# Performance work log

Measured on AMD Instinct MI355X. Metric: run time of the kernel, lower is better.

## Reference

```python
import jax, jax.numpy as jnp
import numpy as np

K = 7          # kernel_size
PAD = K // 2
NAZ, NEL = 12, 5
HID = 64
IC = 2         # input_channels == num_instruments
OC = 2         # output_channels (stereo)
EPS = 1e-5


def conv1d_same(x, w, b):
    # x: (N, Cin, T), w: (Cout, Cin, K) -> (N, Cout, T); cross-correlation like torch
    y = jax.lax.conv_general_dilated(x, w, (1,), 'SAME',
                                     dimension_numbers=('NCH', 'OIH', 'NCH'))
    return y + b[None, :, None]


def batchnorm(x, g, bt):
    # training-mode BatchNorm1d: biased batch stats over (N, T)
    mean = x.mean(axis=(0, 2), keepdims=True)
    var = x.var(axis=(0, 2), keepdims=True)
    return (x - mean) * jax.lax.rsqrt(var + EPS) * g[None, :, None] + bt[None, :, None]


def lrelu(x):
    return jnp.where(x >= 0, x, 0.2 * x)


def setup_inputs() -> dict:
    key = jax.random.key(0)
    ks = jax.random.split(key, 16)
    d = {}
    d['x'] = jax.random.normal(ks[0], (8, IC, 131072), dtype=jnp.float32)
    # spatial_param_net
    d['W1'] = jax.random.normal(ks[1], (HID, IC, K), dtype=jnp.float32) * 0.1
    d['b1'] = jnp.zeros((HID,), jnp.float32)
    d['g1'] = jnp.ones((HID,), jnp.float32)
    d['be1'] = jnp.zeros((HID,), jnp.float32)
    d['W2'] = jax.random.normal(ks[2], (2 * HID, HID, K), dtype=jnp.float32) * 0.05
    d['b2'] = jnp.zeros((2 * HID,), jnp.float32)
    d['g2'] = jnp.ones((2 * HID,), jnp.float32)
    d['be2'] = jnp.zeros((2 * HID,), jnp.float32)
    d['W3'] = jax.random.normal(ks[3], (IC * 3, 2 * HID, K), dtype=jnp.float32) * 0.05
    d['b3'] = jnp.zeros((IC * 3,), jnp.float32)
    # HRTF table: (num_azimuth*num_elevation, output_channels, K)
    d['hrtf'] = jax.random.normal(ks[4], (NAZ * NEL, OC, K), dtype=jnp.float32)
    # binaural_renderer (first conv in-channels = input_channels = 2)
    d['RW1'] = jax.random.normal(ks[5], (HID, IC, K), dtype=jnp.float32) * 0.1
    d['rb1'] = jnp.zeros((HID,), jnp.float32)
    d['rg1'] = jnp.ones((HID,), jnp.float32)
    d['rbe1'] = jnp.zeros((HID,), jnp.float32)
    d['RW2'] = jax.random.normal(ks[6], (2 * HID, HID, K), dtype=jnp.float32) * 0.05
    d['rb2'] = jnp.zeros((2 * HID,), jnp.float32)
    d['rg2'] = jnp.ones((2 * HID,), jnp.float32)
    d['rbe2'] = jnp.zeros((2 * HID,), jnp.float32)
    d['RW3'] = jax.random.normal(ks[7], (OC, 2 * HID, K), dtype=jnp.float32) * 0.05
    d['rb3'] = jnp.zeros((OC,), jnp.float32)
    return d


def reference(x, W1, b1, g1, be1, W2, b2, g2, be2, W3, b3, hrtf,
              RW1, rb1, rg1, rbe1, RW2, rb2, rg2, rbe2, RW3, rb3):
    B, I, T = x.shape
    # spatial parameter network
    h = lrelu(batchnorm(conv1d_same(x, W1, b1), g1, be1))
    h = lrelu(batchnorm(conv1d_same(h, W2, b2), g2, be2))
    sp = jnp.tanh(conv1d_same(h, W3, b3)).reshape(B, I, 3, T)
    # only t=0 of azimuth/elevation/distance is used (matches torch loop)
    az = (sp[:, :, 0, 0] + 1.0) * 0.5 * (NAZ - 1)
    el = (sp[:, :, 1, 0] + 1.0) * 0.5 * (NEL - 1)
    dist = (sp[:, :, 2, 0] + 1.0) * 0.5 * 0.9 + 0.1      # (B, I)
    az_i = jnp.clip(az.astype(jnp.int32), 0, NAZ - 1)
    el_i = jnp.clip(el.astype(jnp.int32), 0, NEL - 1)
    idx = el_i * NAZ + az_i                               # (B, I)
    wg = hrtf[idx]                                        # (B, I, OC, K) gathered filters
    # per-(b,i) conv1d with its gathered HRTF filter, scale by distance, sum over instruments
    xp = jnp.pad(x, ((0, 0), (0, 0), (PAD, PAD)))
    windows = jnp.stack([xp[:, :, k:k + T] for k in range(K)], axis=2)  # (B, I, K, T)
    summed = jnp.einsum('bikt,bick,bi->bct', windows, wg, dist)          # (B, OC, T)
    # binaural renderer
    h = lrelu(batchnorm(conv1d_same(summed, RW1, rb1), rg1, rbe1))
    h = lrelu(batchnorm(conv1d_same(h, RW2, rb2), rg2, rbe2))
    return jnp.tanh(conv1d_same(h, RW3, rb3))
```

## Files before the change

kernel.cpp:

```cpp
#include <hip/hip_runtime.h>
#include <hip/hip_fp16.h>
#include <cstddef>


#define TLEN 131072
#define NB 8
#define NICH 2
#define NHID 64
#define NH2 128
#define EPSV 1e-5f
#define CNTF 1048576.0f
#define FT 120
#define FGRID 1093
#define XCH 2048

typedef _Float16 f16x8 __attribute__((ext_vector_type(8)));
typedef float f32x4 __attribute__((ext_vector_type(4)));

__device__ __forceinline__ float lrelu(float v) { return fmaxf(v, 0.2f * v); }
__device__ __forceinline__ unsigned short h16(float v) {
  return __half_as_ushort(__float2half(v));
}
__device__ __forceinline__ float fh16(unsigned short u) {
  return __half2float(__ushort_as_half(u));
}
__device__ __forceinline__ float ftanh(float x) {
  float e = __expf(2.f * x);
  return 1.f - 2.f / (e + 1.f);
}

__global__ __launch_bounds__(256) void prep_weights(
    const float* __restrict__ W2c, const float* __restrict__ RW2c,
    const float* __restrict__ RW3c,
    const float* __restrict__ W1c, const float* __restrict__ RW1c,
    unsigned short* __restrict__ w2sp, unsigned short* __restrict__ w2re,
    unsigned short* __restrict__ w3g,
    unsigned short* __restrict__ w1sp, unsigned short* __restrict__ w1re)
{
  int e = blockIdx.x * 256 + threadIdx.x;
  if (e < 114688) {
    int e2 = (e >= 57344) ? e - 57344 : e;
    int frag = e2 >> 9, within = e2 & 511;
    int c = frag >> 3, mt = frag & 7;
    int mn = within >> 5, kk = within & 31;
    int o = mt * 16 + mn;
    int tap = c >> 1, ch = (c & 1) * 32 + kk;
    const float* src = (e >= 57344) ? RW2c : W2c;
    unsigned short* dst = (e >= 57344) ? w2re : w2sp;
    dst[e2] = h16(src[(o * 64 + ch) * 7 + tap]);
  } else if (e < 116736) {
    int e2 = e - 114688;
    int c = e2 >> 9, within = e2 & 511;
    int m = within >> 5, kk = within & 31;
    int ch = c * 32 + kk;
    w3g[e2] = (m < 14) ? h16(RW3c[((m / 7) * 128 + ch) * 7 + (m % 7)])
                       : (unsigned short)0;
  } else if (e < 120832) {
    int e2 = e - 116736;
    int which = (e2 >= 2048);
    int e3 = e2 & 2047;
    int m = e3 >> 9, w = e3 & 511;
    int mn = w >> 5, K = w & 31;
    int i = K >> 4, kk = K & 15;
    const float* src = which ? RW1c : W1c;
    unsigned short* dst = which ? w1re : w1sp;
    dst[e3] = (kk < 7) ? h16(src[(m * 16 + mn) * 14 + i * 7 + kk])
                       : (unsigned short)0;
  }
}

__global__ __launch_bounds__(256) void xcorr_stats(
    const float* __restrict__ z, float* __restrict__ partials)
{
  const int b = blockIdx.x >> 6;
  const int t0 = (blockIdx.x & 63) * XCH;
  __shared__ float zs[2][XCH + 8];
  __shared__ float redx[4][30];
  for (int i = 0; i < 2; ++i)
    for (int j = threadIdx.x; j < XCH + 7; j += 256) {
      int tg = t0 + j;
      zs[i][j] = (tg < TLEN) ? z[(b * 2 + i) * TLEN + tg] : 0.f;
    }
  __syncthreads();

  float acc[30];
  #pragma unroll
  for (int q = 0; q < 30; ++q) acc[q] = 0.f;
  const int tb = threadIdx.x * 8;
  #pragma unroll
  for (int tt = 0; tt < 8; ++tt) {
    int j = tb + tt;
    float z0 = zs[0][j], z1 = zs[1][j];
    acc[28] += z0; acc[29] += z1;
    #pragma unroll
    for (int d = 0; d < 7; ++d) {
      float a0 = zs[0][j + d], a1 = zs[1][j + d];
      acc[d]      += z0 * a0;
      acc[7 + d]  += z0 * a1;
      acc[14 + d] += z1 * a0;
      acc[21 + d] += z1 * a1;
    }
  }
  #pragma unroll
  for (int q = 0; q < 30; ++q)
    #pragma unroll
    for (int m = 1; m <= 32; m <<= 1)
      acc[q] += __shfl_xor(acc[q], m, 64);
  const int lane = threadIdx.x & 63, wv = threadIdx.x >> 6;
  if (lane == 0)
    #pragma unroll
    for (int q = 0; q < 30; ++q) redx[wv][q] = acc[q];
  __syncthreads();
  if (threadIdx.x < 30)
    partials[blockIdx.x * 30 + threadIdx.x] =
        redx[0][threadIdx.x] + redx[1][threadIdx.x] +
        redx[2][threadIdx.x] + redx[3][threadIdx.x];
}

__global__ __launch_bounds__(256) void assemble_coef1(
    const float* __restrict__ partials, int nblocks,
    const float* __restrict__ W1c, const float* __restrict__ b1c,
    const float* __restrict__ g, const float* __restrict__ be,
    float* __restrict__ coef)
{
  __shared__ float R[30];
  __shared__ float pr[8][30];
  __shared__ float w1s[64 * 14];
  for (int e = threadIdx.x; e < 64 * 14; e += 256) w1s[e] = W1c[e];
  if (threadIdx.x < 240) {
    int q = threadIdx.x % 30, chunk = threadIdx.x / 30;
    float s = 0.f;
    for (int j = chunk; j < nblocks; j += 8) s += partials[j * 30 + q];
    pr[chunk][q] = s;
  }
  __syncthreads();
  if (threadIdx.x < 30) {
    float s = 0.f;
    #pragma unroll
    for (int c = 0; c < 8; ++c) s += pr[c][threadIdx.x];
    R[threadIdx.x] = s;
  }
  __syncthreads();
  if (threadIdx.x < 64) {
    int o = threadIdx.x;
    const float* w = &w1s[o * 14];
    float b1v = b1c[o];
    float sy = 0.f;
    #pragma unroll
    for (int i = 0; i < 2; ++i)
      #pragma unroll
      for (int k = 0; k < 7; ++k) sy += w[i * 7 + k] * R[28 + i];
    float syy = 0.f;
    #pragma unroll
    for (int i = 0; i < 2; ++i)
      #pragma unroll
      for (int k = 0; k < 7; ++k) {
        float wv = w[i * 7 + k];
        #pragma unroll
        for (int i2 = 0; i2 < 2; ++i2)
          #pragma unroll
          for (int k2 = 0; k2 < 7; ++k2) {
            int d = k2 - k;
            float r = (d >= 0) ? R[i * 14 + i2 * 7 + d]
                               : R[i2 * 14 + i * 7 - d];
            syy += wv * w[i2 * 7 + k2] * r;
          }
      }
    float S1 = CNTF * b1v + sy;
    float S2 = 2.f * b1v * S1 - CNTF * b1v * b1v + syy;
    float mean = S1 / CNTF;
    float var = S2 / CNTF - mean * mean;
    float a = g[o] * rsqrtf(var + EPSV);
    coef[o] = a;
    coef[64 + o] = be[o] - mean * a;
  }
}

__global__ __launch_bounds__(256) void reduce_coef(
    const float* __restrict__ partials, int nblocks, int C,
    const float* __restrict__ bso,
    const float* __restrict__ g, const float* __restrict__ be,
    float* __restrict__ coef)
{
  const int c = blockIdx.x;
  float s = 0.f, ss = 0.f;
  for (int j = threadIdx.x; j < nblocks; j += 256) {
    s  += partials[j * 2 * C + c];
    ss += partials[j * 2 * C + C + c];
  }
  #pragma unroll
  for (int off = 32; off >= 1; off >>= 1) {
    s  += __shfl_down(s, off, 64);
    ss += __shfl_down(ss, off, 64);
  }
  __shared__ float rs[4], rss[4];
  const int lane = threadIdx.x & 63, wv = threadIdx.x >> 6;
  if (lane == 0) { rs[wv] = s; rss[wv] = ss; }
  __syncthreads();
  if (threadIdx.x == 0) {
    float st  = rs[0] + rs[1] + rs[2] + rs[3];
    float sst = rss[0] + rss[1] + rss[2] + rss[3];
    float mean = st / CNTF;
    float var  = sst / CNTF - mean * mean;
    float a = g[c] * rsqrtf(var + EPSV);
    float d = be[c] - mean * a;
    coef[c] = a;
    coef[C + c] = d;
    coef[2 * C + c] = d + a * bso[c];
  }
}

__device__ __forceinline__ void stage_x(
    int t0, int xoff, const float* __restrict__ xin, int b, float* xs)
{
  for (int e = threadIdx.x; e < 2 * 168; e += 256) {
    int i = e / 168, j = e % 168;
    int tg = t0 - xoff + j;
    xs[e] = (tg >= 0 && tg < TLEN) ? xin[(b * NICH + i) * TLEN + tg] : 0.f;
  }
}

template<int HOF>
__device__ __forceinline__ void h1_mfma(
    int t0, const float* xs, unsigned short* xw,
    const unsigned short* __restrict__ w1f,
    const float* __restrict__ coef1, const float* __restrict__ b1c,
    unsigned short* h1f)
{
  for (int e = threadIdx.x; e < 144 * 2; e += 256) {
    int n = e >> 1, i = e & 1;
    const float* xp = &xs[i * 168 + n];
    unsigned short hv[7];
    #pragma unroll
    for (int kk = 0; kk < 7; ++kk) hv[kk] = h16(xp[kk]);
    *(uint4*)(xw + n * 32 + i * 16) = make_uint4(
        hv[0] | ((unsigned)hv[1] << 16), hv[2] | ((unsigned)hv[3] << 16),
        hv[4] | ((unsigned)hv[5] << 16), (unsigned)hv[6]);
    *(uint4*)(xw + n * 32 + i * 16 + 8) = make_uint4(0, 0, 0, 0);
  }
  __syncthreads();

  const int lane = threadIdx.x & 63;
  const int wv = threadIdx.x >> 6;
  const int mn = lane & 15, quad = lane >> 4;
  f16x8 A1 = *(const f16x8*)(w1f + wv * 512 + mn * 32 + quad * 8);
  f32x4 acc1[9];
  #pragma unroll
  for (int nt = 0; nt < 9; ++nt) {
    f32x4 z = {0.f, 0.f, 0.f, 0.f};
    acc1[nt] = z;
  }
  #pragma unroll
  for (int nt = 0; nt < 9; ++nt) {
    f16x8 bb = *(const f16x8*)(xw + (nt * 16 + mn) * 32 + quad * 8);
    acc1[nt] = __builtin_amdgcn_mfma_f32_16x16x32_f16(A1, bb, acc1[nt], 0, 0, 0);
  }
  const int ch0 = wv * 16 + quad * 4;
  float a1v[4], dd[4];
  #pragma unroll
  for (int r = 0; r < 4; ++r) {
    a1v[r] = coef1[ch0 + r];
    dd[r]  = coef1[64 + ch0 + r] + a1v[r] * b1c[ch0 + r];
  }
  #pragma unroll
  for (int nt = 0; nt < 9; ++nt) {
    int n = nt * 16 + mn;
    int t = t0 - HOF + n;
    bool ok = (t >= 0) && (t < TLEN);
    unsigned us[4];
    #pragma unroll
    for (int r = 0; r < 4; ++r) {
      float v = lrelu(a1v[r] * acc1[nt][r] + dd[r]);
      us[r] = h16(ok ? v : 0.f);
    }
    *(uint2*)(h1f + n * 72 + ch0) =
        make_uint2(us[0] | (us[1] << 16), us[2] | (us[3] << 16));
  }
}

template<int SAVE>
__global__ __launch_bounds__(256, 4) void conv2_stats_mfma(
    const float* __restrict__ xin,
    const unsigned short* __restrict__ w1f, const float* __restrict__ b1c,
    const float* __restrict__ coef1,
    const unsigned short* __restrict__ w2f,
    const float* __restrict__ b2c,
    float* __restrict__ partials,
    unsigned short* __restrict__ h1out)
{
  const int b  = blockIdx.x >> 10;
  const int t0 = (blockIdx.x & 1023) * 128;

  __shared__ __align__(16) char smem[31296];
  unsigned short* h1f = (unsigned short*)smem;
  float* xs = (float*)(smem + 20736);
  unsigned short* xw = (unsigned short*)(smem + 22080);
  float* redS = (float*)smem;
  float* redSS= (float*)(smem + 8704);

  stage_x(t0, 6, xin, b, xs);
  __syncthreads();
  h1_mfma<3>(t0, xs, xw, w1f, coef1, b1c, h1f);
  __syncthreads();

  const int lane = threadIdx.x & 63;
  const int wv = threadIdx.x >> 6;
  const int mn = lane & 15, quad = lane >> 4;

  f32x4 acc[2][8];
  #pragma unroll
  for (int mt = 0; mt < 2; ++mt)
    #pragma unroll
    for (int nt = 0; nt < 8; ++nt) {
      f32x4 z = {0.f, 0.f, 0.f, 0.f};
      acc[mt][nt] = z;
    }

  f16x8 ca[2], na[2];
  auto loadA = [&](int c, f16x8 (&A)[2]) {
    #pragma unroll
    for (int mt = 0; mt < 2; ++mt)
      A[mt] = *(const f16x8*)(w2f + (c * 8 + wv * 2 + mt) * 512 + mn * 32 + quad * 8);
  };
  loadA(0, ca);
  #pragma unroll
  for (int c = 0; c < 14; ++c) {
    if (c < 13) loadA(c + 1, na);
    const int tap = c >> 1;
    const int ch0 = (c & 1) * 32 + quad * 8;
    #pragma unroll
    for (int nt = 0; nt < 8; ++nt) {
      f16x8 bb = *(const f16x8*)(h1f + (nt * 16 + mn + tap) * 72 + ch0);
      acc[0][nt] = __builtin_amdgcn_mfma_f32_16x16x32_f16(ca[0], bb, acc[0][nt], 0, 0, 0);
      acc[1][nt] = __builtin_amdgcn_mfma_f32_16x16x32_f16(ca[1], bb, acc[1][nt], 0, 0, 0);
    }
    ca[0] = na[0]; ca[1] = na[1];
  }

  if (SAVE == 1) {
    for (int e = threadIdx.x; e < 1024; e += 256) {
      int row = e >> 3, c8 = (e & 7) * 8;
      *(uint4*)(h1out + ((size_t)(b * TLEN + t0 + row) * 64 + c8)) =
          *(const uint4*)(h1f + (row + 3) * 72 + c8);
    }
  }
  __syncthreads();

  #pragma unroll
  for (int mt = 0; mt < 2; ++mt)
    #pragma unroll
    for (int r = 0; r < 4; ++r) {
      int o = (wv * 2 + mt) * 16 + quad * 4 + r;
      float bo = b2c[o];
      float s = 0.f, ss = 0.f;
      #pragma unroll
      for (int nt = 0; nt < 8; ++nt) {
        float v = acc[mt][nt][r] + bo;
        s += v; ss += v * v;
      }
      redS[o * 17 + mn] = s;
      redSS[o * 17 + mn] = ss;
    }
  __syncthreads();
  {
    int o = threadIdx.x & 127;
    const float* src = (threadIdx.x < 128) ? redS : redSS;
    float s = 0.f;
    #pragma unroll
    for (int j = 0; j < 16; ++j) s += src[o * 17 + j];
    partials[blockIdx.x * 256 + threadIdx.x] = s;
  }
}

__global__ __launch_bounds__(256) void finalize_spatial(
    const float* __restrict__ x,
    const float* __restrict__ W1c, const float* __restrict__ b1c,
    const float* __restrict__ coef1,
    const float* __restrict__ W2c, const float* __restrict__ b2c,
    const float* __restrict__ coef2,
    const float* __restrict__ W3c, const float* __restrict__ b3c,
    const float* __restrict__ hrtf, float* __restrict__ wgbuf)
{
  __shared__ float xl[NB * 2 * 16];
  __shared__ float h1l[NB * 64 * 10];
  __shared__ float h2l[NB * NH2 * 4];
  __shared__ float sp[48];
  const int tid = threadIdx.x;
  {
    int bb = tid >> 5, i = (tid >> 4) & 1, j = tid & 15;
    int t = j - 6;
    xl[tid] = (t >= 0) ? x[(bb * 2 + i) * TLEN + t] : 0.f;
  }
  __syncthreads();
  for (int e = tid; e < NB * 64; e += 256) {
    int bb = e >> 6, ch = e & 63;
    float a1 = coef1[ch], d1 = coef1[64 + ch], bo = b1c[ch];
    for (int tt = 0; tt < 10; ++tt) {
      float acc = bo;
      #pragma unroll
      for (int i2 = 0; i2 < 2; ++i2)
        #pragma unroll
        for (int k = 0; k < 7; ++k)
          acc += xl[(bb * 2 + i2) * 16 + tt + k] * W1c[ch * 14 + i2 * 7 + k];
      float v = lrelu(a1 * acc + d1);
      h1l[(bb * 64 + ch) * 10 + tt] = (tt >= 3) ? v : 0.f;
    }
  }
  __syncthreads();
  for (int e = tid; e < NB * NH2; e += 256) {
    int bb = e >> 7, o = e & 127;
    float a2 = coef2[o], d2 = coef2[NH2 + o], bo = b2c[o];
    float acc[4] = {bo, bo, bo, bo};
    for (int i = 0; i < 64; ++i)
      #pragma unroll
      for (int k = 0; k < 7; ++k) {
        float w = W2c[(o * 64 + i) * 7 + k];
        #pragma unroll
        for (int t = 0; t < 4; ++t)
          acc[t] += h1l[(bb * 64 + i) * 10 + t + k] * w;
      }
    #pragma unroll
    for (int t = 0; t < 4; ++t)
      h2l[(bb * NH2 + o) * 4 + t] = lrelu(a2 * acc[t] + d2);
  }
  __syncthreads();
  if (tid < 48) {
    int bb = tid / 6, c3 = tid % 6;
    float acc = b3c[c3];
    for (int c = 0; c < NH2; ++c)
      #pragma unroll
      for (int k = 3; k < 7; ++k)
        acc += h2l[(bb * NH2 + c) * 4 + (k - 3)] * W3c[(c3 * NH2 + c) * 7 + k];
    sp[tid] = tanhf(acc);
  }
  __syncthreads();
  if (tid < 16) {
    int bb = tid >> 1, i = tid & 1;
    float az = (sp[bb * 6 + i * 3 + 0] + 1.f) * 0.5f * 11.f;
    float el = (sp[bb * 6 + i * 3 + 1] + 1.f) * 0.5f * 4.f;
    float dist = (sp[bb * 6 + i * 3 + 2] + 1.f) * 0.5f * 0.9f + 0.1f;
    int azi = min(max((int)az, 0), 11);
    int eli = min(max((int)el, 0), 4);
    int idx = eli * 12 + azi;
    for (int e = 0; e < 14; ++e)
      wgbuf[(bb * 2 + i) * 14 + e] = hrtf[idx * 14 + e] * dist;
  }
}

__global__ __launch_bounds__(256) void mix_kernel(
    const float* __restrict__ x, const float* __restrict__ wgbuf,
    float* __restrict__ summed)
{
  const int b = blockIdx.x >> 7;
  const int t0 = (blockIdx.x & 127) * 1024 + threadIdx.x * 4;
  float wv[2][2][7];
  #pragma unroll
  for (int i = 0; i < 2; ++i)
    #pragma unroll
    for (int c = 0; c < 2; ++c)
      #pragma unroll
      for (int k = 0; k < 7; ++k)
        wv[i][c][k] = wgbuf[(b * 2 + i) * 14 + c * 7 + k];
  float acc[2][4] = {{0.f, 0.f, 0.f, 0.f}, {0.f, 0.f, 0.f, 0.f}};
  #pragma unroll
  for (int i = 0; i < 2; ++i) {
    float xl[12];
    #pragma unroll
    for (int j = 0; j < 12; ++j) {
      int tg = t0 - 4 + j;
      xl[j] = (tg >= 0 && tg < TLEN) ? x[(b * 2 + i) * TLEN + tg] : 0.f;
    }
    #pragma unroll
    for (int c = 0; c < 2; ++c)
      #pragma unroll
      for (int k = 0; k < 7; ++k)
        #pragma unroll
        for (int tt = 0; tt < 4; ++tt)
          acc[c][tt] += xl[tt + k + 1] * wv[i][c][k];
  }
  #pragma unroll
  for (int c = 0; c < 2; ++c)
    *reinterpret_cast<float4*>(&summed[(b * 2 + c) * TLEN + t0]) =
        make_float4(acc[c][0], acc[c][1], acc[c][2], acc[c][3]);
}

__device__ __forceinline__ void final_tail(
    int b, int t0, f32x4 (&acc)[2][8],
    const float* __restrict__ coef2,
    const unsigned short* __restrict__ w3g, const float* __restrict__ rb3c,
    unsigned short* h2t, unsigned short* dq, float* __restrict__ out)
{
  const int lane = threadIdx.x & 63;
  const int wv = threadIdx.x >> 6;
  const int mn = lane & 15, quad = lane >> 4;

  float a2v[2][4], dd2[2][4];
  #pragma unroll
  for (int mt = 0; mt < 2; ++mt)
    #pragma unroll
    for (int r = 0; r < 4; ++r) {
      int o = (wv * 2 + mt) * 16 + quad * 4 + r;
      a2v[mt][r] = coef2[o];
      dd2[mt][r] = coef2[2 * NH2 + o];
    }
  __syncthreads();

  #pragma unroll
  for (int nt = 0; nt < 8; ++nt) {
    int jp = nt * 16 + mn;
    int t = t0 - 3 + jp;
    bool ok = (t >= 0) && (t < TLEN);
    #pragma unroll
    for (int mt = 0; mt < 2; ++mt) {
      int obase = (wv * 2 + mt) * 16 + quad * 4;
      unsigned us[4];
      #pragma unroll
      for (int r = 0; r < 4; ++r) {
        float v = lrelu(a2v[mt][r] * acc[mt][nt][r] + dd2[mt][r]);
        us[r] = h16(ok ? v : 0.f);
      }
      *(uint2*)(h2t + jp * 136 + obase) =
          make_uint2(us[0] | (us[1] << 16), us[2] | (us[3] << 16));
    }
  }
  __syncthreads();

  const int nt0 = wv * 2;
  f32x4 acc3[2];
  #pragma unroll
  for (int i = 0; i < 2; ++i) {
    f32x4 z = {0.f, 0.f, 0.f, 0.f};
    acc3[i] = z;
  }
  #pragma unroll
  for (int c = 0; c < 4; ++c) {
    f16x8 A3 = *(const f16x8*)(w3g + c * 512 + mn * 32 + quad * 8);
    #pragma unroll
    for (int i = 0; i < 2; ++i) {
      f16x8 bb = *(const f16x8*)(h2t + ((nt0 + i) * 16 + mn) * 136 + c * 32 + quad * 8);
      acc3[i] = __builtin_amdgcn_mfma_f32_16x16x32_f16(A3, bb, acc3[i], 0, 0, 0);
    }
  }
  #pragma unroll
  for (int i = 0; i < 2; ++i) {
    int n = (nt0 + i) * 16 + mn;
    unsigned us[4];
    #pragma unroll
    for (int r = 0; r < 4; ++r) us[r] = h16(acc3[i][r]);
    *(uint2*)(dq + n * 20 + quad * 4) =
        make_uint2(us[0] | (us[1] << 16), us[2] | (us[3] << 16));
  }
  __syncthreads();

  {
    int tid = threadIdx.x;
    if (tid < 240) {
      int oc = (tid >= FT) ? 1 : 0;
      int u = tid - oc * FT;
      float s = rb3c[oc];
      #pragma unroll
      for (int tap = 0; tap < 7; ++tap)
        s += fh16(dq[(u + tap) * 20 + oc * 7 + tap]);
      int t = t0 + u;
      if (t < TLEN) out[(b * 2 + oc) * TLEN + t] = ftanh(s);
    }
  }
}

__device__ __forceinline__ void conv2_loop(
    const unsigned short* h1f, const unsigned short* __restrict__ w2f,
    f32x4 (&acc)[2][8])
{
  const int lane = threadIdx.x & 63;
  const int wv = threadIdx.x >> 6;
  const int mn = lane & 15, quad = lane >> 4;
  #pragma unroll
  for (int mt = 0; mt < 2; ++mt)
    #pragma unroll
    for (int nt = 0; nt < 8; ++nt) {
      f32x4 z = {0.f, 0.f, 0.f, 0.f};
      acc[mt][nt] = z;
    }
  f16x8 ca[2], na[2];
  auto loadA = [&](int c, f16x8 (&A)[2]) {
    #pragma unroll
    for (int mt = 0; mt < 2; ++mt)
      A[mt] = *(const f16x8*)(w2f + (c * 8 + wv * 2 + mt) * 512 + mn * 32 + quad * 8);
  };
  loadA(0, ca);
  #pragma unroll
  for (int c = 0; c < 14; ++c) {
    if (c < 13) loadA(c + 1, na);
    const int tap = c >> 1;
    const int ch0 = (c & 1) * 32 + quad * 8;
    #pragma unroll
    for (int nt = 0; nt < 8; ++nt) {
      f16x8 bb = *(const f16x8*)(h1f + (nt * 16 + mn + tap) * 72 + ch0);
      acc[0][nt] = __builtin_amdgcn_mfma_f32_16x16x32_f16(ca[0], bb, acc[0][nt], 0, 0, 0);
      acc[1][nt] = __builtin_amdgcn_mfma_f32_16x16x32_f16(ca[1], bb, acc[1][nt], 0, 0, 0);
    }
    ca[0] = na[0]; ca[1] = na[1];
  }
}

__global__ __launch_bounds__(256, 4) void conv2_final_mfma(
    const float* __restrict__ xin,
    const unsigned short* __restrict__ w1f, const float* __restrict__ b1c,
    const float* __restrict__ coef1,
    const unsigned short* __restrict__ w2f,
    const float* __restrict__ coef2,
    const unsigned short* __restrict__ w3g, const float* __restrict__ rb3c,
    float* __restrict__ out)
{
  const int b  = blockIdx.y;
  const int t0 = blockIdx.x * FT;

  __shared__ __align__(16) char smem[39936];
  unsigned short* h1f = (unsigned short*)smem;
  float* xs = (float*)(smem + 20736);
  unsigned short* xw = (unsigned short*)(smem + 22080);
  unsigned short* h2t = (unsigned short*)smem;
  unsigned short* dq  = (unsigned short*)(smem + 34816);

  stage_x(t0, 9, xin, b, xs);
  __syncthreads();
  h1_mfma<6>(t0, xs, xw, w1f, coef1, b1c, h1f);
  __syncthreads();

  f32x4 acc[2][8];
  conv2_loop(h1f, w2f, acc);
  final_tail(b, t0, acc, coef2, w3g, rb3c, h2t, dq, out);
}

__global__ __launch_bounds__(256, 4) void conv2_final_h1(
    const unsigned short* __restrict__ h1g,
    const unsigned short* __restrict__ w2f,
    const float* __restrict__ coef2,
    const unsigned short* __restrict__ w3g, const float* __restrict__ rb3c,
    float* __restrict__ out)
{
  const int b  = blockIdx.y;
  const int t0 = blockIdx.x * FT;

  __shared__ __align__(16) char smem[39936];
  unsigned short* h1f = (unsigned short*)smem;
  unsigned short* h2t = (unsigned short*)smem;
  unsigned short* dq  = (unsigned short*)(smem + 34816);

  for (int e = threadIdx.x; e < 144 * 8; e += 256) {
    int r = e >> 3, c8 = (e & 7) * 8;
    int t = t0 - 6 + r;
    uint4 v = make_uint4(0, 0, 0, 0);
    if (t >= 0 && t < TLEN)
      v = *(const uint4*)(h1g + ((size_t)(b * TLEN + t) * 64 + c8));
    *(uint4*)(h1f + r * 72 + c8) = v;
  }
  __syncthreads();

  f32x4 acc[2][8];
  conv2_loop(h1f, w2f, acc);
  final_tail(b, t0, acc, coef2, w3g, rb3c, h2t, dq, out);
}

extern "C" void kernel_launch(void* const* d_in, const int* in_sizes, int n_in,
                              void* d_out, int out_size, void* d_ws, size_t ws_size,
                              hipStream_t stream)
{
  (void)in_sizes; (void)n_in; (void)out_size;
  const float* x    = (const float*)d_in[0];
  const float* W1   = (const float*)d_in[1];
  const float* b1   = (const float*)d_in[2];
  const float* g1   = (const float*)d_in[3];
  const float* be1  = (const float*)d_in[4];
  const float* W2   = (const float*)d_in[5];
  const float* b2   = (const float*)d_in[6];
  const float* g2   = (const float*)d_in[7];
  const float* be2  = (const float*)d_in[8];
  const float* W3   = (const float*)d_in[9];
  const float* b3   = (const float*)d_in[10];
  const float* hrtf = (const float*)d_in[11];
  const float* RW1  = (const float*)d_in[12];
  const float* rb1  = (const float*)d_in[13];
  const float* rg1  = (const float*)d_in[14];
  const float* rbe1 = (const float*)d_in[15];
  const float* RW2  = (const float*)d_in[16];
  const float* rb2  = (const float*)d_in[17];
  const float* rg2  = (const float*)d_in[18];
  const float* rbe2 = (const float*)d_in[19];
  const float* RW3  = (const float*)d_in[20];
  const float* rb3  = (const float*)d_in[21];
  float* out = (float*)d_out;

  float* partialsB = (float*)d_out;

  char* ws = (char*)d_ws;
  float* partialsA      = (float*)(ws + 0);
  float* summed         = (float*)(ws + 524288);
  float* coef1          = (float*)(ws + 8912896);
  float* coef2          = (float*)(ws + 8913408);
  float* coefR1         = (float*)(ws + 8914944);
  float* coefR2         = (float*)(ws + 8915456);
  float* wgbuf          = (float*)(ws + 8916992);
  unsigned short* w2sp  = (unsigned short*)(ws + 8918016);
  unsigned short* w2re  = (unsigned short*)(ws + 9032704);
  unsigned short* w3g   = (unsigned short*)(ws + 9147392);
  unsigned short* w1sp  = (unsigned short*)(ws + 9151488);
  unsigned short* w1re  = (unsigned short*)(ws + 9155584);
  unsigned short* h1g   = (unsigned short*)(ws + 16777216);
  const size_t WS_NEEDED_MID = 16777216ull + 134217728ull;
  const bool mid = ws_size >= WS_NEEDED_MID;

  prep_weights<<<472, 256, 0, stream>>>(W2, RW2, RW3, W1, RW1,
                                        w2sp, w2re, w3g, w1sp, w1re);
  xcorr_stats<<<512, 256, 0, stream>>>(x, partialsA);
  assemble_coef1<<<1, 256, 0, stream>>>(partialsA, 512, W1, b1, g1, be1, coef1);
  conv2_stats_mfma<0><<<8192, 256, 0, stream>>>(x, w1sp, b1, coef1, w2sp,
                                                b2, partialsB, nullptr);
  reduce_coef<<<128, 256, 0, stream>>>(partialsB, 8192, 128, b2, g2, be2, coef2);
  finalize_spatial<<<1, 256, 0, stream>>>(x, W1, b1, coef1, W2, b2, coef2,
                                          W3, b3, hrtf, wgbuf);
  mix_kernel<<<1024, 256, 0, stream>>>(x, wgbuf, summed);
  xcorr_stats<<<512, 256, 0, stream>>>(summed, partialsA);
  assemble_coef1<<<1, 256, 0, stream>>>(partialsA, 512, RW1, rb1, rg1, rbe1, coefR1);
  if (mid) {
    conv2_stats_mfma<1><<<8192, 256, 0, stream>>>(summed, w1re, rb1, coefR1,
                                                  w2re, rb2, partialsB, h1g);
  } else {
    conv2_stats_mfma<0><<<8192, 256, 0, stream>>>(summed, w1re, rb1, coefR1,
                                                  w2re, rb2, partialsB, nullptr);
  }
  reduce_coef<<<128, 256, 0, stream>>>(partialsB, 8192, 128, rb2, rg2, rbe2, coefR2);
  if (mid) {
    conv2_final_h1<<<dim3(FGRID, NB), 256, 0, stream>>>(
        h1g, w2re, coefR2, w3g, rb3, out);
  } else {
    conv2_final_mfma<<<dim3(FGRID, NB), 256, 0, stream>>>(
        summed, w1re, rb1, coefR1, w2re, coefR2, w3g, rb3, out);
  }
}
```

Baseline: 655.4 us.

## Fuse HRTF mix with renderer input cross-correlation stats; parallelize spatial finalize

```diff
diff --git a/kernel.cpp b/kernel.cpp
--- a/kernel.cpp
+++ b/kernel.cpp
@@ -303,46 +303,46 @@
   h1_mfma<3>(t0, xs, xw, w1f, coef1, b1c, h1f);
   __syncthreads();
 
-  const int lane = threadIdx.x & 63;
-  const int wv = threadIdx.x >> 6;
-  const int mn = lane & 15, quad = lane >> 4;
-
-  f32x4 acc[2][8];
-  #pragma unroll
-  for (int mt = 0; mt < 2; ++mt)
-    #pragma unroll
-    for (int nt = 0; nt < 8; ++nt) {
-      f32x4 z = {0.f, 0.f, 0.f, 0.f};
-      acc[mt][nt] = z;
-    }
-
-  f16x8 ca[2], na[2];
-  auto loadA = [&](int c, f16x8 (&A)[2]) {
-    #pragma unroll
-    for (int mt = 0; mt < 2; ++mt)
-      A[mt] = *(const f16x8*)(w2f + (c * 8 + wv * 2 + mt) * 512 + mn * 32 + quad * 8);
-  };
-  loadA(0, ca);
-  #pragma unroll
-  for (int c = 0; c < 14; ++c) {
-    if (c < 13) loadA(c + 1, na);
-    const int tap = c >> 1;
-    const int ch0 = (c & 1) * 32 + quad * 8;
-    #pragma unroll
-    for (int nt = 0; nt < 8; ++nt) {
-      f16x8 bb = *(const f16x8*)(h1f + (nt * 16 + mn + tap) * 72 + ch0);
-      acc[0][nt] = __builtin_amdgcn_mfma_f32_16x16x32_f16(ca[0], bb, acc[0][nt], 0, 0, 0);
-      acc[1][nt] = __builtin_amdgcn_mfma_f32_16x16x32_f16(ca[1], bb, acc[1][nt], 0, 0, 0);
-    }
-    ca[0] = na[0]; ca[1] = na[1];
-  }
-
   if (SAVE == 1) {
     for (int e = threadIdx.x; e < 1024; e += 256) {
       int row = e >> 3, c8 = (e & 7) * 8;
       *(uint4*)(h1out + ((size_t)(b * TLEN + t0 + row) * 64 + c8)) =
           *(const uint4*)(h1f + (row + 3) * 72 + c8);
     }
+  }
+
+  const int lane = threadIdx.x & 63;
+  const int wv = threadIdx.x >> 6;
+  const int mn = lane & 15, quad = lane >> 4;
+
+  f32x4 acc[2][8];
+  #pragma unroll
+  for (int mt = 0; mt < 2; ++mt)
+    #pragma unroll
+    for (int nt = 0; nt < 8; ++nt) {
+      f32x4 z = {0.f, 0.f, 0.f, 0.f};
+      acc[mt][nt] = z;
+    }
+
+  f16x8 ca[2], na[2];
+  auto loadA = [&](int c, f16x8 (&A)[2]) {
+    #pragma unroll
+    for (int mt = 0; mt < 2; ++mt)
+      A[mt] = *(const f16x8*)(w2f + (c * 8 + wv * 2 + mt) * 512 + mn * 32 + quad * 8);
+  };
+  loadA(0, ca);
+  #pragma unroll
+  for (int c = 0; c < 14; ++c) {
+    if (c < 13) loadA(c + 1, na);
+    const int tap = c >> 1;
+    const int ch0 = (c & 1) * 32 + quad * 8;
+    #pragma unroll
+    for (int nt = 0; nt < 8; ++nt) {
+      f16x8 bb = *(const f16x8*)(h1f + (nt * 16 + mn + tap) * 72 + ch0);
+      acc[0][nt] = __builtin_amdgcn_mfma_f32_16x16x32_f16(ca[0], bb, acc[0][nt], 0, 0, 0);
+      acc[1][nt] = __builtin_amdgcn_mfma_f32_16x16x32_f16(ca[1], bb, acc[1][nt], 0, 0, 0);
+    }
+    ca[0] = na[0]; ca[1] = na[1];
   }
   __syncthreads();
 
@@ -381,19 +381,20 @@
     const float* __restrict__ W3c, const float* __restrict__ b3c,
     const float* __restrict__ hrtf, float* __restrict__ wgbuf)
 {
-  __shared__ float xl[NB * 2 * 16];
-  __shared__ float h1l[NB * 64 * 10];
-  __shared__ float h2l[NB * NH2 * 4];
-  __shared__ float sp[48];
+  const int bb = blockIdx.x;
+  __shared__ float xl[2 * 16];
+  __shared__ float h1l[64 * 10];
+  __shared__ float h2l[NH2 * 4];
+  __shared__ float sp[6];
   const int tid = threadIdx.x;
-  {
-    int bb = tid >> 5, i = (tid >> 4) & 1, j = tid & 15;
+  if (tid < 32) {
+    int i = tid >> 4, j = tid & 15;
     int t = j - 6;
     xl[tid] = (t >= 0) ? x[(bb * 2 + i) * TLEN + t] : 0.f;
   }
   __syncthreads();
-  for (int e = tid; e < NB * 64; e += 256) {
-    int bb = e >> 6, ch = e & 63;
+  if (tid < 64) {
+    int ch = tid;
     float a1 = coef1[ch], d1 = coef1[64 + ch], bo = b1c[ch];
     for (int tt = 0; tt < 10; ++tt) {
       float acc = bo;
@@ -401,14 +402,14 @@
       for (int i2 = 0; i2 < 2; ++i2)
         #pragma unroll
         for (int k = 0; k < 7; ++k)
-          acc += xl[(bb * 2 + i2) * 16 + tt + k] * W1c[ch * 14 + i2 * 7 + k];
+          acc += xl[i2 * 16 + tt + k] * W1c[ch * 14 + i2 * 7 + k];
       float v = lrelu(a1 * acc + d1);
-      h1l[(bb * 64 + ch) * 10 + tt] = (tt >= 3) ? v : 0.f;
-    }
-  }
-  __syncthreads();
-  for (int e = tid; e < NB * NH2; e += 256) {
-    int bb = e >> 7, o = e & 127;
+      h1l[ch * 10 + tt] = (tt >= 3) ? v : 0.f;
+    }
+  }
+  __syncthreads();
+  if (tid < NH2) {
+    int o = tid;
     float a2 = coef2[o], d2 = coef2[NH2 + o], bo = b2c[o];
     float acc[4] = {bo, bo, bo, bo};
     for (int i = 0; i < 64; ++i)
@@ -417,28 +418,28 @@
         float w = W2c[(o * 64 + i) * 7 + k];
         #pragma unroll
         for (int t = 0; t < 4; ++t)
-          acc[t] += h1l[(bb * 64 + i) * 10 + t + k] * w;
+          acc[t] += h1l[i * 10 + t + k] * w;
       }
     #pragma unroll
     for (int t = 0; t < 4; ++t)
-      h2l[(bb * NH2 + o) * 4 + t] = lrelu(a2 * acc[t] + d2);
-  }
-  __syncthreads();
-  if (tid < 48) {
-    int bb = tid / 6, c3 = tid % 6;
+      h2l[o * 4 + t] = lrelu(a2 * acc[t] + d2);
+  }
+  __syncthreads();
+  if (tid < 6) {
+    int c3 = tid;
     float acc = b3c[c3];
     for (int c = 0; c < NH2; ++c)
       #pragma unroll
       for (int k = 3; k < 7; ++k)
-        acc += h2l[(bb * NH2 + c) * 4 + (k - 3)] * W3c[(c3 * NH2 + c) * 7 + k];
-    sp[tid] = tanhf(acc);
-  }
-  __syncthreads();
-  if (tid < 16) {
-    int bb = tid >> 1, i = tid & 1;
-    float az = (sp[bb * 6 + i * 3 + 0] + 1.f) * 0.5f * 11.f;
-    float el = (sp[bb * 6 + i * 3 + 1] + 1.f) * 0.5f * 4.f;
-    float dist = (sp[bb * 6 + i * 3 + 2] + 1.f) * 0.5f * 0.9f + 0.1f;
+        acc += h2l[c * 4 + (k - 3)] * W3c[(c3 * NH2 + c) * 7 + k];
+    sp[c3] = tanhf(acc);
+  }
+  __syncthreads();
+  if (tid < 2) {
+    int i = tid;
+    float az = (sp[i * 3 + 0] + 1.f) * 0.5f * 11.f;
+    float el = (sp[i * 3 + 1] + 1.f) * 0.5f * 4.f;
+    float dist = (sp[i * 3 + 2] + 1.f) * 0.5f * 0.9f + 0.1f;
     int azi = min(max((int)az, 0), 11);
     int eli = min(max((int)el, 0), 4);
     int idx = eli * 12 + azi;
@@ -447,12 +448,15 @@
   }
 }
 
-__global__ __launch_bounds__(256) void mix_kernel(
+__global__ __launch_bounds__(256) void mix_xcorr(
     const float* __restrict__ x, const float* __restrict__ wgbuf,
-    float* __restrict__ summed)
-{
-  const int b = blockIdx.x >> 7;
-  const int t0 = (blockIdx.x & 127) * 1024 + threadIdx.x * 4;
+    float* __restrict__ summed, float* __restrict__ partials)
+{
+  const int b = blockIdx.x >> 6;
+  const int t0 = (blockIdx.x & 63) * XCH;
+  __shared__ float zs[2][XCH + 8];
+  __shared__ float redx[4][30];
+
   float wv[2][2][7];
   #pragma unroll
   for (int i = 0; i < 2; ++i)
@@ -461,27 +465,90 @@
       #pragma unroll
       for (int k = 0; k < 7; ++k)
         wv[i][c][k] = wgbuf[(b * 2 + i) * 14 + c * 7 + k];
-  float acc[2][4] = {{0.f, 0.f, 0.f, 0.f}, {0.f, 0.f, 0.f, 0.f}};
-  #pragma unroll
-  for (int i = 0; i < 2; ++i) {
-    float xl[12];
-    #pragma unroll
-    for (int j = 0; j < 12; ++j) {
-      int tg = t0 - 4 + j;
-      xl[j] = (tg >= 0 && tg < TLEN) ? x[(b * 2 + i) * TLEN + tg] : 0.f;
-    }
+
+  const int tb = threadIdx.x * 8;
+  {
+    float acc[2][8];
     #pragma unroll
     for (int c = 0; c < 2; ++c)
       #pragma unroll
-      for (int k = 0; k < 7; ++k)
+      for (int tt = 0; tt < 8; ++tt) acc[c][tt] = 0.f;
+    #pragma unroll
+    for (int i = 0; i < 2; ++i) {
+      float xl[14];
+      #pragma unroll
+      for (int j = 0; j < 14; ++j) {
+        int tg = t0 + tb - 3 + j;
+        xl[j] = (tg >= 0 && tg < TLEN) ? x[(b * 2 + i) * TLEN + tg] : 0.f;
+      }
+      #pragma unroll
+      for (int c = 0; c < 2; ++c)
         #pragma unroll
-        for (int tt = 0; tt < 4; ++tt)
-          acc[c][tt] += xl[tt + k + 1] * wv[i][c][k];
-  }
-  #pragma unroll
-  for (int c = 0; c < 2; ++c)
-    *reinterpret_cast<float4*>(&summed[(b * 2 + c) * TLEN + t0]) =
-        make_float4(acc[c][0], acc[c][1], acc[c][2], acc[c][3]);
+        for (int k = 0; k < 7; ++k)
+          #pragma unroll
+          for (int tt = 0; tt < 8; ++tt)
+            acc[c][tt] += xl[tt + k] * wv[i][c][k];
+    }
+    #pragma unroll
+    for (int c = 0; c < 2; ++c) {
+      #pragma unroll
+      for (int tt = 0; tt < 8; ++tt) zs[c][tb + tt] = acc[c][tt];
+      *reinterpret_cast<float4*>(&summed[(b * 2 + c) * TLEN + t0 + tb]) =
+          make_float4(acc[c][0], acc[c][1], acc[c][2], acc[c][3]);
+      *reinterpret_cast<float4*>(&summed[(b * 2 + c) * TLEN + t0 + tb + 4]) =
+          make_float4(acc[c][4], acc[c][5], acc[c][6], acc[c][7]);
+    }
+  }
+  if (threadIdx.x < 7) {
+    int t = t0 + XCH + threadIdx.x;
+    float s0 = 0.f, s1 = 0.f;
+    if (t < TLEN) {
+      #pragma unroll
+      for (int i = 0; i < 2; ++i)
+        #pragma unroll
+        for (int k = 0; k < 7; ++k) {
+          int tg = t + k - 3;
+          float xv = (tg >= 0 && tg < TLEN) ? x[(b * 2 + i) * TLEN + tg] : 0.f;
+          s0 += xv * wv[i][0][k];
+          s1 += xv * wv[i][1][k];
+        }
+    }
+    zs[0][XCH + threadIdx.x] = s0;
+    zs[1][XCH + threadIdx.x] = s1;
+  }
+  __syncthreads();
+
+  float acc[30];
+  #pragma unroll
+  for (int q = 0; q < 30; ++q) acc[q] = 0.f;
+  #pragma unroll
+  for (int tt = 0; tt < 8; ++tt) {
+    int j = tb + tt;
+    float z0 = zs[0][j], z1 = zs[1][j];
+    acc[28] += z0; acc[29] += z1;
+    #pragma unroll
+    for (int d = 0; d < 7; ++d) {
+      float a0 = zs[0][j + d], a1 = zs[1][j + d];
+      acc[d]      += z0 * a0;
+      acc[7 + d]  += z0 * a1;
+      acc[14 + d] += z1 * a0;
+      acc[21 + d] += z1 * a1;
+    }
+  }
+  #pragma unroll
+  for (int q = 0; q < 30; ++q)
+    #pragma unroll
+    for (int m = 1; m <= 32; m <<= 1)
+      acc[q] += __shfl_xor(acc[q], m, 64);
+  const int lane = threadIdx.x & 63, wvx = threadIdx.x >> 6;
+  if (lane == 0)
+    #pragma unroll
+    for (int q = 0; q < 30; ++q) redx[wvx][q] = acc[q];
+  __syncthreads();
+  if (threadIdx.x < 30)
+    partials[blockIdx.x * 30 + threadIdx.x] =
+        redx[0][threadIdx.x] + redx[1][threadIdx.x] +
+        redx[2][threadIdx.x] + redx[3][threadIdx.x];
 }
 
 __device__ __forceinline__ void final_tail(
@@ -717,10 +784,9 @@
   conv2_stats_mfma<0><<<8192, 256, 0, stream>>>(x, w1sp, b1, coef1, w2sp,
                                                 b2, partialsB, nullptr);
   reduce_coef<<<128, 256, 0, stream>>>(partialsB, 8192, 128, b2, g2, be2, coef2);
-  finalize_spatial<<<1, 256, 0, stream>>>(x, W1, b1, coef1, W2, b2, coef2,
+  finalize_spatial<<<8, 256, 0, stream>>>(x, W1, b1, coef1, W2, b2, coef2,
                                           W3, b3, hrtf, wgbuf);
-  mix_kernel<<<1024, 256, 0, stream>>>(x, wgbuf, summed);
-  xcorr_stats<<<512, 256, 0, stream>>>(summed, partialsA);
+  mix_xcorr<<<512, 256, 0, stream>>>(x, wgbuf, summed, partialsA);
   assemble_coef1<<<1, 256, 0, stream>>>(partialsA, 512, RW1, rb1, rg1, rbe1, coefR1);
   if (mid) {
     conv2_stats_mfma<1><<<8192, 256, 0, stream>>>(summed, w1re, rb1, coefR1,
```

Measured after the change: 603.0 us. 8.0% less time.
